# Kernel tuning notes

Measured on AMD Instinct MI355X. Metric: run time of the kernel, lower is better.

The kernel has to match this reference:

```python
import jax, jax.numpy as jnp
import numpy as np


def setup_inputs() -> dict:
    key = jax.random.key(0)
    kq, kk, kv = jax.random.split(key, 3)
    B, M, QT, KVT, H = 2, 16, 2048, 2048, 128
    q = jax.random.normal(kq, (B, M, QT, H), dtype=jnp.float32)
    k = jax.random.normal(kk, (B, M, KVT, H), dtype=jnp.float32)
    v = jax.random.normal(kv, (B, M, KVT, H), dtype=jnp.float32)
    return {"q": q, "k": k, "v": v}


def reference(q, k, v):
    # QKBmm: broadcast-multiply + sum == einsum contraction over H.
    # NOTE: original module applies NO 1/sqrt(H) scaling.
    score = jnp.einsum("bmqh,bmkh->bmqk", q, k)  # [B,M,QT,KVT]
    score = jax.nn.softmax(score, axis=-1)
    # SVBmm: broadcast-multiply + sum over KVT.
    out = jnp.einsum("bmqk,bmkh->bmqh", score, v)  # [B,M,QT,H]
    return out
```

## Files before the change

kernel.cpp:

```cpp
#include <hip/hip_runtime.h>
#include <hip/hip_bf16.h>
#include <math.h>


#define HD     128
#define QTL    2048
#define KVTL   2048
#define NHEAD  32
#define KVBLK  64
#define NKT    (KVTL / KVBLK)
#define QBLKB  128
#define TILE_BYTES 32768
#define WS_NEEDED ((size_t)NHEAD * NKT * TILE_BYTES)

using f32x4  = __attribute__((ext_vector_type(4))) float;
using f32x16 = __attribute__((ext_vector_type(16))) float;
using f16x8  = __attribute__((ext_vector_type(8))) _Float16;
using i32x2  = __attribute__((ext_vector_type(2))) int;
using i32x4  = __attribute__((ext_vector_type(4))) int;
using bf16x8 = __attribute__((ext_vector_type(8))) __bf16;
using bf16x4 = __attribute__((ext_vector_type(4))) __bf16;

#define NK_CHUNK (NHEAD * NKT * 64 * 16)
#define NV_CHUNK (NHEAD * NKT * 8 * 128)

__global__ __launch_bounds__(256) void sdpa_prep(const float* __restrict__ kg,
                                                 const float* __restrict__ vg,
                                                 char* __restrict__ ws)
{
    const int idx = blockIdx.x * 256 + threadIdx.x;
    if (idx < NK_CHUNK) {
        const int s    = idx & 15;
        const int r    = (idx >> 4) & 63;
        const int kt   = (idx >> 10) & 31;
        const int head = idx >> 15;
        const int c    = s ^ (r & 15);
        const float* src = kg + ((size_t)head * KVTL + kt * 64 + r) * HD + c * 8;
        float4 a = *(const float4*)src;
        float4 b = *(const float4*)(src + 4);
        f16x8 h8;
        h8[0] = (_Float16)a.x; h8[1] = (_Float16)a.y;
        h8[2] = (_Float16)a.z; h8[3] = (_Float16)a.w;
        h8[4] = (_Float16)b.x; h8[5] = (_Float16)b.y;
        h8[6] = (_Float16)b.z; h8[7] = (_Float16)b.w;
        char* base = ws + (size_t)(head * NKT + kt) * TILE_BYTES;
        *(f16x8*)(base + r * 256 + s * 16) = h8;
    } else if (idx < NK_CHUNK + NV_CHUNK) {
        const int j    = idx - NK_CHUNK;
        const int h    = j & 127;
        const int c    = (j >> 7) & 7;
        const int kt   = (j >> 10) & 31;
        const int head = j >> 15;
        const int rr   = h & 63;
        const int u    = h >> 6;
        const int s    = (u * 8 + c) ^ (rr & 15);
        const float* src = vg + ((size_t)head * KVTL + kt * 64 + c * 8) * HD + h;
        f16x8 o;
        #pragma unroll
        for (int i = 0; i < 8; ++i)
            o[i] = (_Float16)src[(size_t)i * HD];
        char* base = ws + (size_t)(head * NKT + kt) * TILE_BYTES;
        *(f16x8*)(base + 16384 + rr * 256 + s * 16) = o;
    }
}

__global__ __launch_bounds__(256, 2) void sdpa_fwd(const float* __restrict__ qg,
                                                   const char* __restrict__ ws,
                                                   float* __restrict__ og)
{
    const int head  = blockIdx.y;
    const int qblk  = blockIdx.x * QBLKB;
    const float* qh = qg + (size_t)head * QTL * HD;
    const char*  wh = ws + (size_t)head * NKT * TILE_BYTES;

    const int t  = threadIdx.x;
    const int wv = t >> 6;
    const int l  = t & 63;
    const int lq = l & 31;
    const int hi = l >> 5;
    const int lm = l & 15;

    __shared__ __align__(16) char arena[65536];

    f16x8 qf[8];
    {
        const float* qrow = qh + (size_t)(qblk + wv * 32 + lq) * HD;
        #pragma unroll
        for (int hs = 0; hs < 8; ++hs) {
            float4 a = *(const float4*)(qrow + hs * 16 + hi * 8);
            float4 b = *(const float4*)(qrow + hs * 16 + hi * 8 + 4);
            f16x8 f;
            f[0] = (_Float16)a.x; f[1] = (_Float16)a.y;
            f[2] = (_Float16)a.z; f[3] = (_Float16)a.w;
            f[4] = (_Float16)b.x; f[5] = (_Float16)b.y;
            f[6] = (_Float16)b.z; f[7] = (_Float16)b.w;
            qf[hs] = f;
        }
    }

    f32x16 acc_o[4];
    #pragma unroll
    for (int ht = 0; ht < 4; ++ht)
        #pragma unroll
        for (int r = 0; r < 16; ++r) acc_o[ht][r] = 0.f;

    float m = -INFINITY, ln = 0.f;
    const float LOG2E = 1.4426950408889634f;

    i32x4 stg[8];

    #pragma unroll
    for (int j = 0; j < 8; ++j)
        stg[j] = *(const i32x4*)(wh + j * 4096 + t * 16);
    #pragma unroll
    for (int j = 0; j < 8; ++j)
        *(i32x4*)(arena + j * 4096 + t * 16) = stg[j];
    __syncthreads();

    for (int kt = 0; kt < NKT; ++kt) {
        const int cur = kt & 1;
        const char* base = arena + cur * 32768;

        if (kt + 1 < NKT) {
            const char* g = wh + (size_t)(kt + 1) * TILE_BYTES;
            #pragma unroll
            for (int j = 0; j < 8; ++j)
                stg[j] = *(const i32x4*)(g + j * 4096 + t * 16);
        }

        f32x16 acc_s[2];
        __builtin_amdgcn_s_setprio(1);
        #pragma unroll
        for (int kk = 0; kk < 2; ++kk) {
            f32x16 acc;
            #pragma unroll
            for (int r = 0; r < 16; ++r) acc[r] = 0.f;
            #pragma unroll
            for (int hs = 0; hs < 8; ++hs) {
                const int off = (kk * 32 + lq) * 256 + (((hs * 2 + hi) ^ lm) * 16);
                f16x8 kf = *(const f16x8*)(base + off);
                acc = __builtin_amdgcn_mfma_f32_32x32x16_f16(kf, qf[hs], acc, 0, 0, 0);
            }
            acc_s[kk] = acc;
        }
        __builtin_amdgcn_s_setprio(0);

        float pm0 = -INFINITY, pm1 = -INFINITY, pm2 = -INFINITY, pm3 = -INFINITY;
        #pragma unroll
        for (int kk = 0; kk < 2; ++kk)
            #pragma unroll
            for (int r = 0; r < 16; r += 4) {
                pm0 = fmaxf(pm0, acc_s[kk][r + 0]);
                pm1 = fmaxf(pm1, acc_s[kk][r + 1]);
                pm2 = fmaxf(pm2, acc_s[kk][r + 2]);
                pm3 = fmaxf(pm3, acc_s[kk][r + 3]);
            }
        float pmax = fmaxf(fmaxf(pm0, pm1), fmaxf(pm2, pm3));
        pmax = fmaxf(pmax, __shfl_xor(pmax, 32));

        if (!__all(pmax <= m + 8.0f)) {
            const float mnew = fmaxf(m, pmax);
            const float sc   = exp2f((m - mnew) * LOG2E);
            m = mnew; ln *= sc;
            #pragma unroll
            for (int ht = 0; ht < 4; ++ht)
                #pragma unroll
                for (int r = 0; r < 16; ++r) acc_o[ht][r] *= sc;
        }

        i32x4 fr[4];
        #pragma unroll
        for (int kk = 0; kk < 2; ++kk) {
            float p[16];
            float s0 = 0.f, s1 = 0.f, s2 = 0.f, s3 = 0.f;
            #pragma unroll
            for (int r = 0; r < 16; r += 4) {
                p[r + 0] = exp2f((acc_s[kk][r + 0] - m) * LOG2E); s0 += p[r + 0];
                p[r + 1] = exp2f((acc_s[kk][r + 1] - m) * LOG2E); s1 += p[r + 1];
                p[r + 2] = exp2f((acc_s[kk][r + 2] - m) * LOG2E); s2 += p[r + 2];
                p[r + 3] = exp2f((acc_s[kk][r + 3] - m) * LOG2E); s3 += p[r + 3];
            }
            ln += (s0 + s1) + (s2 + s3);
            int t01 = __builtin_bit_cast(int, __builtin_amdgcn_cvt_pkrtz(p[0],  p[1]));
            int t23 = __builtin_bit_cast(int, __builtin_amdgcn_cvt_pkrtz(p[2],  p[3]));
            int t45 = __builtin_bit_cast(int, __builtin_amdgcn_cvt_pkrtz(p[4],  p[5]));
            int t67 = __builtin_bit_cast(int, __builtin_amdgcn_cvt_pkrtz(p[6],  p[7]));
            int t89 = __builtin_bit_cast(int, __builtin_amdgcn_cvt_pkrtz(p[8],  p[9]));
            int tAB = __builtin_bit_cast(int, __builtin_amdgcn_cvt_pkrtz(p[10], p[11]));
            int tCD = __builtin_bit_cast(int, __builtin_amdgcn_cvt_pkrtz(p[12], p[13]));
            int tEF = __builtin_bit_cast(int, __builtin_amdgcn_cvt_pkrtz(p[14], p[15]));
            i32x2 sw;
            sw = __builtin_amdgcn_permlane32_swap(t01, t45, false, false);
            fr[2*kk][0] = sw[0]; fr[2*kk][2] = sw[1];
            sw = __builtin_amdgcn_permlane32_swap(t23, t67, false, false);
            fr[2*kk][1] = sw[0]; fr[2*kk][3] = sw[1];
            sw = __builtin_amdgcn_permlane32_swap(t89, tCD, false, false);
            fr[2*kk+1][0] = sw[0]; fr[2*kk+1][2] = sw[1];
            sw = __builtin_amdgcn_permlane32_swap(tAB, tEF, false, false);
            fr[2*kk+1][1] = sw[0]; fr[2*kk+1][3] = sw[1];
        }

        const char* Vb = base + 16384;
        __builtin_amdgcn_s_setprio(1);
        #pragma unroll
        for (int ht = 0; ht < 4; ++ht) {
            #pragma unroll
            for (int ks = 0; ks < 4; ++ks) {
                const int off = ((ht & 1) * 32 + lq) * 256 +
                                ((((ht >> 1) * 8 + ks * 2 + hi) ^ lm) * 16);
                f16x8 vf = *(const f16x8*)(Vb + off);
                acc_o[ht] = __builtin_amdgcn_mfma_f32_32x32x16_f16(
                    vf, __builtin_bit_cast(f16x8, fr[ks]), acc_o[ht], 0, 0, 0);
            }
        }
        __builtin_amdgcn_s_setprio(0);

        if (kt + 1 < NKT) {
            char* nbuf = arena + (cur ^ 1) * 32768;
            #pragma unroll
            for (int j = 0; j < 8; ++j)
                *(i32x4*)(nbuf + j * 4096 + t * 16) = stg[j];
        }

        __syncthreads();
    }

    ln += __shfl_xor(ln, 32);
    const float inv = 1.f / ln;

    __syncthreads();
    const int qloc = wv * 32 + lq;
    #pragma unroll
    for (int ht = 0; ht < 4; ++ht) {
        #pragma unroll
        for (int r = 0; r < 4; ++r) {
            f32x4 v;
            v[0] = acc_o[ht][4*r+0] * inv;
            v[1] = acc_o[ht][4*r+1] * inv;
            v[2] = acc_o[ht][4*r+2] * inv;
            v[3] = acc_o[ht][4*r+3] * inv;
            const int slot = ht * 8 + 2 * r + hi;
            *(f32x4*)(arena + qloc * 512 + ((slot ^ lq) * 16)) = v;
        }
    }
    __syncthreads();
    {
        float* ob = og + (size_t)(head * QTL + qblk) * HD;
        #pragma unroll
        for (int j = 0; j < 16; ++j) {
            const int n  = j * 256 + t;
            const int qr = n >> 5;
            const int sl = n & 31;
            f32x4 v = *(const f32x4*)(arena + qr * 512 + ((sl ^ (qr & 31)) * 16));
            *(f32x4*)(ob + (size_t)qr * HD + sl * 4) = v;
        }
    }
}

__global__ __launch_bounds__(256) void sdpa_fwd_v1(const float* __restrict__ qg,
                                                   const float* __restrict__ kg,
                                                   const float* __restrict__ vg,
                                                   float* __restrict__ og)
{
    const int head  = blockIdx.y;
    const int qbase = blockIdx.x * 64;
    const float* qh = qg + (size_t)head * QTL * HD;
    const float* kh = kg + (size_t)head * KVTL * HD;
    const float* vh = vg + (size_t)head * KVTL * HD;
    float*       oh = og + (size_t)head * QTL * HD;

    const int t  = threadIdx.x;
    const int wv = t >> 6;
    const int l  = t & 63;
    const int lr = l & 15;
    const int lg = l >> 4;

    __shared__ __bf16 Kth[32][HD + 8];
    __shared__ __bf16 Ktl[32][HD + 8];
    __shared__ __bf16 Vt[HD][32 + 8];
    __shared__ __bf16 Pw[4][16][32 + 8];

    bf16x8 qfh[4], qfl[4];
    {
        const float* qrow = qh + (size_t)(qbase + wv * 16 + lr) * HD;
        #pragma unroll
        for (int ks = 0; ks < 4; ++ks) {
            bf16x8 fh, fl;
            #pragma unroll
            for (int i = 0; i < 8; ++i) {
                float x = qrow[ks * 32 + lg * 8 + i];
                __bf16 h = (__bf16)x;
                fh[i] = h;
                fl[i] = (__bf16)(x - (float)h);
            }
            qfh[ks] = fh; qfl[ks] = fl;
        }
    }

    f32x4 acc_o[8];
    #pragma unroll
    for (int h8 = 0; h8 < 8; ++h8) acc_o[h8] = (f32x4){0.f, 0.f, 0.f, 0.f};
    float mrow[4], lrow[4];
    #pragma unroll
    for (int r = 0; r < 4; ++r) { mrow[r] = -INFINITY; lrow[r] = 0.f; }
    const float LOG2E = 1.4426950408889634f;

    for (int kt = 0; kt < 64; ++kt) {
        const float* kbase = kh + (size_t)kt * 32 * HD;
        const float* vbase = vh + (size_t)kt * 32 * HD;
        __syncthreads();
        #pragma unroll
        for (int j = 0; j < 4; ++j) {
            const int e   = (j * 256 + t) * 4;
            const int row = e >> 7;
            const int col = e & 127;
            float4 f = *(const float4*)(kbase + e);
            bf16x4 h4, l4;
            h4[0] = (__bf16)f.x; l4[0] = (__bf16)(f.x - (float)h4[0]);
            h4[1] = (__bf16)f.y; l4[1] = (__bf16)(f.y - (float)h4[1]);
            h4[2] = (__bf16)f.z; l4[2] = (__bf16)(f.z - (float)h4[2]);
            h4[3] = (__bf16)f.w; l4[3] = (__bf16)(f.w - (float)h4[3]);
            *(bf16x4*)&Kth[row][col] = h4;
            *(bf16x4*)&Ktl[row][col] = l4;
        }
        #pragma unroll
        for (int j = 0; j < 4; ++j) {
            const int n     = t & 127;
            const int strip = (t >> 7) + 2 * j;
            bf16x4 b4;
            #pragma unroll
            for (int i = 0; i < 4; ++i)
                b4[i] = (__bf16)vbase[(size_t)(4 * strip + i) * HD + n];
            *(bf16x4*)&Vt[n][4 * strip] = b4;
        }
        __syncthreads();

        f32x4 acc_s[2];
        #pragma unroll
        for (int nt = 0; nt < 2; ++nt) {
            acc_s[nt] = (f32x4){0.f, 0.f, 0.f, 0.f};
            #pragma unroll
            for (int ks = 0; ks < 4; ++ks) {
                bf16x8 kh8 = *(const bf16x8*)&Kth[nt * 16 + lr][ks * 32 + lg * 8];
                bf16x8 kl8 = *(const bf16x8*)&Ktl[nt * 16 + lr][ks * 32 + lg * 8];
                acc_s[nt] = __builtin_amdgcn_mfma_f32_16x16x32_bf16(qfh[ks], kh8, acc_s[nt], 0, 0, 0);
                acc_s[nt] = __builtin_amdgcn_mfma_f32_16x16x32_bf16(qfl[ks], kh8, acc_s[nt], 0, 0, 0);
                acc_s[nt] = __builtin_amdgcn_mfma_f32_16x16x32_bf16(qfh[ks], kl8, acc_s[nt], 0, 0, 0);
            }
        }
        float p[2][4];
        #pragma unroll
        for (int r = 0; r < 4; ++r) {
            float vm = fmaxf(acc_s[0][r], acc_s[1][r]);
            vm = fmaxf(vm, __shfl_xor(vm, 1));
            vm = fmaxf(vm, __shfl_xor(vm, 2));
            vm = fmaxf(vm, __shfl_xor(vm, 4));
            vm = fmaxf(vm, __shfl_xor(vm, 8));
            const float mnew  = fmaxf(mrow[r], vm);
            const float scale = exp2f((mrow[r] - mnew) * LOG2E);
            mrow[r] = mnew;
            float ps = 0.f;
            #pragma unroll
            for (int nt = 0; nt < 2; ++nt) {
                float pe = exp2f((acc_s[nt][r] - mnew) * LOG2E);
                p[nt][r] = pe; ps += pe;
            }
            lrow[r] = lrow[r] * scale + ps;
            #pragma unroll
            for (int h8 = 0; h8 < 8; ++h8) acc_o[h8][r] *= scale;
        }
        #pragma unroll
        for (int nt = 0; nt < 2; ++nt)
            #pragma unroll
            for (int r = 0; r < 4; ++r)
                Pw[wv][lg * 4 + r][nt * 16 + lr] = (__bf16)p[nt][r];
        bf16x8 pf = *(const bf16x8*)&Pw[wv][lr][lg * 8];
        #pragma unroll
        for (int h8 = 0; h8 < 8; ++h8) {
            bf16x8 vf = *(const bf16x8*)&Vt[h8 * 16 + lr][lg * 8];
            acc_o[h8] = __builtin_amdgcn_mfma_f32_16x16x32_bf16(pf, vf, acc_o[h8], 0, 0, 0);
        }
    }
    float invl[4];
    #pragma unroll
    for (int r = 0; r < 4; ++r) {
        float s = lrow[r];
        s += __shfl_xor(s, 1);
        s += __shfl_xor(s, 2);
        s += __shfl_xor(s, 4);
        s += __shfl_xor(s, 8);
        invl[r] = 1.f / s;
    }
    float* ob = oh + (size_t)(qbase + wv * 16) * HD;
    #pragma unroll
    for (int h8 = 0; h8 < 8; ++h8)
        #pragma unroll
        for (int r = 0; r < 4; ++r)
            ob[(size_t)(lg * 4 + r) * HD + h8 * 16 + lr] = acc_o[h8][r] * invl[r];
}

extern "C" void kernel_launch(void* const* d_in, const int* in_sizes, int n_in,
                              void* d_out, int out_size, void* d_ws, size_t ws_size,
                              hipStream_t stream) {
    const float* q = (const float*)d_in[0];
    const float* k = (const float*)d_in[1];
    const float* v = (const float*)d_in[2];
    float* out = (float*)d_out;

    if (ws_size >= WS_NEEDED) {
        char* ws = (char*)d_ws;
        const int total_chunks = NK_CHUNK + NV_CHUNK;
        sdpa_prep<<<total_chunks / 256, 256, 0, stream>>>(k, v, ws);
        dim3 grid(QTL / QBLKB, NHEAD, 1);
        sdpa_fwd<<<grid, dim3(256, 1, 1), 0, stream>>>(q, ws, out);
    } else {
        dim3 grid(QTL / 64, NHEAD, 1);
        sdpa_fwd_v1<<<grid, dim3(256, 1, 1), 0, stream>>>(q, k, v, out);
    }
}
```

Measured before the change: 115.9 us.

## Use 512-thread blocks over 256 query rows with 128-key double-buffered tiles

Each block now has 8 waves covering 256 query rows, where before it had 4 waves over 128 rows. Each loop iteration stages a 128-key K/V tile (two 64-key subtiles) into 128KB of double-buffered dynamic LDS, and the online softmax runs per 32-key chunk inside the iteration. This halves both the number of times each K/V tile is copied from global memory into LDS and the number of block barriers per key. In exchange, occupancy drops to one large block per CU with only 256 blocks in the grid. It also relies on the device accepting a 128KB dynamic shared-memory launch.

```diff
diff --git a/kernel.cpp b/kernel.cpp
--- a/kernel.cpp
+++ b/kernel.cpp
@@ -7,11 +7,12 @@
 #define QTL    2048
 #define KVTL   2048
 #define NHEAD  32
-#define KVBLK  64
-#define NKT    (KVTL / KVBLK)
-#define QBLKB  128
-#define TILE_BYTES 32768
-#define WS_NEEDED ((size_t)NHEAD * NKT * TILE_BYTES)
+#define NKT64  32
+#define NITER  16
+#define QBLKB  256
+#define SUB_BYTES  32768
+#define TILE2_BYTES 65536
+#define WS_NEEDED ((size_t)NHEAD * NKT64 * SUB_BYTES)
 
 using f32x4  = __attribute__((ext_vector_type(4))) float;
 using f32x16 = __attribute__((ext_vector_type(16))) float;
@@ -21,8 +22,8 @@
 using bf16x8 = __attribute__((ext_vector_type(8))) __bf16;
 using bf16x4 = __attribute__((ext_vector_type(4))) __bf16;
 
-#define NK_CHUNK (NHEAD * NKT * 64 * 16)
-#define NV_CHUNK (NHEAD * NKT * 8 * 128)
+#define NK_CHUNK (NHEAD * NKT64 * 64 * 16)
+#define NV_CHUNK (NHEAD * NKT64 * 8 * 128)
 
 __global__ __launch_bounds__(256) void sdpa_prep(const float* __restrict__ kg,
                                                  const float* __restrict__ vg,
@@ -43,7 +44,7 @@
         h8[2] = (_Float16)a.z; h8[3] = (_Float16)a.w;
         h8[4] = (_Float16)b.x; h8[5] = (_Float16)b.y;
         h8[6] = (_Float16)b.z; h8[7] = (_Float16)b.w;
-        char* base = ws + (size_t)(head * NKT + kt) * TILE_BYTES;
+        char* base = ws + (size_t)(head * NKT64 + kt) * SUB_BYTES;
         *(f16x8*)(base + r * 256 + s * 16) = h8;
     } else if (idx < NK_CHUNK + NV_CHUNK) {
         const int j    = idx - NK_CHUNK;
@@ -59,19 +60,21 @@
         #pragma unroll
         for (int i = 0; i < 8; ++i)
             o[i] = (_Float16)src[(size_t)i * HD];
-        char* base = ws + (size_t)(head * NKT + kt) * TILE_BYTES;
+        char* base = ws + (size_t)(head * NKT64 + kt) * SUB_BYTES;
         *(f16x8*)(base + 16384 + rr * 256 + s * 16) = o;
     }
 }
 
-__global__ __launch_bounds__(256, 2) void sdpa_fwd(const float* __restrict__ qg,
+__global__ __launch_bounds__(512, 1) void sdpa_fwd(const float* __restrict__ qg,
                                                    const char* __restrict__ ws,
                                                    float* __restrict__ og)
 {
+    extern __shared__ __align__(16) char arena[];
+
     const int head  = blockIdx.y;
     const int qblk  = blockIdx.x * QBLKB;
     const float* qh = qg + (size_t)head * QTL * HD;
-    const char*  wh = ws + (size_t)head * NKT * TILE_BYTES;
+    const char*  wh = ws + (size_t)head * NKT64 * SUB_BYTES;
 
     const int t  = threadIdx.x;
     const int wv = t >> 6;
@@ -79,8 +82,6 @@
     const int lq = l & 31;
     const int hi = l >> 5;
     const int lm = l & 15;
-
-    __shared__ __align__(16) char arena[65536];
 
     f16x8 qf[8];
     {
@@ -108,118 +109,111 @@
     const float LOG2E = 1.4426950408889634f;
 
     i32x4 stg[8];
-
     #pragma unroll
     for (int j = 0; j < 8; ++j)
-        stg[j] = *(const i32x4*)(wh + j * 4096 + t * 16);
+        stg[j] = *(const i32x4*)(wh + j * 8192 + t * 16);
     #pragma unroll
     for (int j = 0; j < 8; ++j)
-        *(i32x4*)(arena + j * 4096 + t * 16) = stg[j];
+        *(i32x4*)(arena + j * 8192 + t * 16) = stg[j];
     __syncthreads();
 
-    for (int kt = 0; kt < NKT; ++kt) {
+    for (int kt = 0; kt < NITER; ++kt) {
         const int cur = kt & 1;
-        const char* base = arena + cur * 32768;
-
-        if (kt + 1 < NKT) {
-            const char* g = wh + (size_t)(kt + 1) * TILE_BYTES;
+        const char* base = arena + cur * TILE2_BYTES;
+
+        if (kt + 1 < NITER) {
+            const char* g = wh + (size_t)(kt + 1) * TILE2_BYTES;
             #pragma unroll
             for (int j = 0; j < 8; ++j)
-                stg[j] = *(const i32x4*)(g + j * 4096 + t * 16);
-        }
-
-        f32x16 acc_s[2];
-        __builtin_amdgcn_s_setprio(1);
-        #pragma unroll
-        for (int kk = 0; kk < 2; ++kk) {
-            f32x16 acc;
-            #pragma unroll
-            for (int r = 0; r < 16; ++r) acc[r] = 0.f;
+                stg[j] = *(const i32x4*)(g + j * 8192 + t * 16);
+        }
+
+        #pragma unroll
+        for (int kk = 0; kk < 4; ++kk) {
+            const char* sub = base + (kk >> 1) * SUB_BYTES;
+
+            f32x16 acc_s;
+            #pragma unroll
+            for (int r = 0; r < 16; ++r) acc_s[r] = 0.f;
+            __builtin_amdgcn_s_setprio(1);
             #pragma unroll
             for (int hs = 0; hs < 8; ++hs) {
-                const int off = (kk * 32 + lq) * 256 + (((hs * 2 + hi) ^ lm) * 16);
-                f16x8 kf = *(const f16x8*)(base + off);
-                acc = __builtin_amdgcn_mfma_f32_32x32x16_f16(kf, qf[hs], acc, 0, 0, 0);
-            }
-            acc_s[kk] = acc;
-        }
-        __builtin_amdgcn_s_setprio(0);
-
-        float pm0 = -INFINITY, pm1 = -INFINITY, pm2 = -INFINITY, pm3 = -INFINITY;
-        #pragma unroll
-        for (int kk = 0; kk < 2; ++kk)
-            #pragma unroll
-            for (int r = 0; r < 16; r += 4) {
-                pm0 = fmaxf(pm0, acc_s[kk][r + 0]);
-                pm1 = fmaxf(pm1, acc_s[kk][r + 1]);
-                pm2 = fmaxf(pm2, acc_s[kk][r + 2]);
-                pm3 = fmaxf(pm3, acc_s[kk][r + 3]);
-            }
-        float pmax = fmaxf(fmaxf(pm0, pm1), fmaxf(pm2, pm3));
-        pmax = fmaxf(pmax, __shfl_xor(pmax, 32));
-
-        if (!__all(pmax <= m + 8.0f)) {
-            const float mnew = fmaxf(m, pmax);
-            const float sc   = exp2f((m - mnew) * LOG2E);
-            m = mnew; ln *= sc;
-            #pragma unroll
-            for (int ht = 0; ht < 4; ++ht)
+                const int off = ((kk & 1) * 32 + lq) * 256 + (((hs * 2 + hi) ^ lm) * 16);
+                f16x8 kf = *(const f16x8*)(sub + off);
+                acc_s = __builtin_amdgcn_mfma_f32_32x32x16_f16(kf, qf[hs], acc_s, 0, 0, 0);
+            }
+            __builtin_amdgcn_s_setprio(0);
+
+            float pm0 = fmaxf(fmaxf(acc_s[0], acc_s[1]), fmaxf(acc_s[2], acc_s[3]));
+            float pm1 = fmaxf(fmaxf(acc_s[4], acc_s[5]), fmaxf(acc_s[6], acc_s[7]));
+            float pm2 = fmaxf(fmaxf(acc_s[8], acc_s[9]), fmaxf(acc_s[10], acc_s[11]));
+            float pm3 = fmaxf(fmaxf(acc_s[12], acc_s[13]), fmaxf(acc_s[14], acc_s[15]));
+            float pmax = fmaxf(fmaxf(pm0, pm1), fmaxf(pm2, pm3));
+            pmax = fmaxf(pmax, __shfl_xor(pmax, 32));
+            if (!__all(pmax <= m + 8.0f)) {
+                const float mnew = fmaxf(m, pmax);
+                const float sc   = exp2f((m - mnew) * LOG2E);
+                m = mnew; ln *= sc;
                 #pragma unroll
-                for (int r = 0; r < 16; ++r) acc_o[ht][r] *= sc;
-        }
-
-        i32x4 fr[4];
-        #pragma unroll
-        for (int kk = 0; kk < 2; ++kk) {
+                for (int ht = 0; ht < 4; ++ht)
+                    #pragma unroll
+                    for (int r = 0; r < 16; ++r) acc_o[ht][r] *= sc;
+            }
+
             float p[16];
-            float s0 = 0.f, s1 = 0.f, s2 = 0.f, s3 = 0.f;
-            #pragma unroll
-            for (int r = 0; r < 16; r += 4) {
-                p[r + 0] = exp2f((acc_s[kk][r + 0] - m) * LOG2E); s0 += p[r + 0];
-                p[r + 1] = exp2f((acc_s[kk][r + 1] - m) * LOG2E); s1 += p[r + 1];
-                p[r + 2] = exp2f((acc_s[kk][r + 2] - m) * LOG2E); s2 += p[r + 2];
-                p[r + 3] = exp2f((acc_s[kk][r + 3] - m) * LOG2E); s3 += p[r + 3];
-            }
-            ln += (s0 + s1) + (s2 + s3);
-            int t01 = __builtin_bit_cast(int, __builtin_amdgcn_cvt_pkrtz(p[0],  p[1]));
-            int t23 = __builtin_bit_cast(int, __builtin_amdgcn_cvt_pkrtz(p[2],  p[3]));
-            int t45 = __builtin_bit_cast(int, __builtin_amdgcn_cvt_pkrtz(p[4],  p[5]));
-            int t67 = __builtin_bit_cast(int, __builtin_amdgcn_cvt_pkrtz(p[6],  p[7]));
-            int t89 = __builtin_bit_cast(int, __builtin_amdgcn_cvt_pkrtz(p[8],  p[9]));
-            int tAB = __builtin_bit_cast(int, __builtin_amdgcn_cvt_pkrtz(p[10], p[11]));
-            int tCD = __builtin_bit_cast(int, __builtin_amdgcn_cvt_pkrtz(p[12], p[13]));
-            int tEF = __builtin_bit_cast(int, __builtin_amdgcn_cvt_pkrtz(p[14], p[15]));
-            i32x2 sw;
-            sw = __builtin_amdgcn_permlane32_swap(t01, t45, false, false);
-            fr[2*kk][0] = sw[0]; fr[2*kk][2] = sw[1];
-            sw = __builtin_amdgcn_permlane32_swap(t23, t67, false, false);
-            fr[2*kk][1] = sw[0]; fr[2*kk][3] = sw[1];
-            sw = __builtin_amdgcn_permlane32_swap(t89, tCD, false, false);
-            fr[2*kk+1][0] = sw[0]; fr[2*kk+1][2] = sw[1];
-            sw = __builtin_amdgcn_permlane32_swap(tAB, tEF, false, false);
-            fr[2*kk+1][1] = sw[0]; fr[2*kk+1][3] = sw[1];
-        }
-
-        const char* Vb = base + 16384;
-        __builtin_amdgcn_s_setprio(1);
-        #pragma unroll
-        for (int ht = 0; ht < 4; ++ht) {
-            #pragma unroll
-            for (int ks = 0; ks < 4; ++ks) {
-                const int off = ((ht & 1) * 32 + lq) * 256 +
-                                ((((ht >> 1) * 8 + ks * 2 + hi) ^ lm) * 16);
-                f16x8 vf = *(const f16x8*)(Vb + off);
-                acc_o[ht] = __builtin_amdgcn_mfma_f32_32x32x16_f16(
-                    vf, __builtin_bit_cast(f16x8, fr[ks]), acc_o[ht], 0, 0, 0);
-            }
-        }
-        __builtin_amdgcn_s_setprio(0);
-
-        if (kt + 1 < NKT) {
-            char* nbuf = arena + (cur ^ 1) * 32768;
+            {
+                float s0 = 0.f, s1 = 0.f, s2 = 0.f, s3 = 0.f;
+                #pragma unroll
+                for (int r = 0; r < 16; r += 4) {
+                    p[r + 0] = exp2f((acc_s[r + 0] - m) * LOG2E); s0 += p[r + 0];
+                    p[r + 1] = exp2f((acc_s[r + 1] - m) * LOG2E); s1 += p[r + 1];
+                    p[r + 2] = exp2f((acc_s[r + 2] - m) * LOG2E); s2 += p[r + 2];
+                    p[r + 3] = exp2f((acc_s[r + 3] - m) * LOG2E); s3 += p[r + 3];
+                }
+                ln += (s0 + s1) + (s2 + s3);
+            }
+            i32x4 fr[2];
+            {
+                int t01 = __builtin_bit_cast(int, __builtin_amdgcn_cvt_pkrtz(p[0],  p[1]));
+                int t23 = __builtin_bit_cast(int, __builtin_amdgcn_cvt_pkrtz(p[2],  p[3]));
+                int t45 = __builtin_bit_cast(int, __builtin_amdgcn_cvt_pkrtz(p[4],  p[5]));
+                int t67 = __builtin_bit_cast(int, __builtin_amdgcn_cvt_pkrtz(p[6],  p[7]));
+                int t89 = __builtin_bit_cast(int, __builtin_amdgcn_cvt_pkrtz(p[8],  p[9]));
+                int tAB = __builtin_bit_cast(int, __builtin_amdgcn_cvt_pkrtz(p[10], p[11]));
+                int tCD = __builtin_bit_cast(int, __builtin_amdgcn_cvt_pkrtz(p[12], p[13]));
+                int tEF = __builtin_bit_cast(int, __builtin_amdgcn_cvt_pkrtz(p[14], p[15]));
+                i32x2 sw;
+                sw = __builtin_amdgcn_permlane32_swap(t01, t45, false, false);
+                fr[0][0] = sw[0]; fr[0][2] = sw[1];
+                sw = __builtin_amdgcn_permlane32_swap(t23, t67, false, false);
+                fr[0][1] = sw[0]; fr[0][3] = sw[1];
+                sw = __builtin_amdgcn_permlane32_swap(t89, tCD, false, false);
+                fr[1][0] = sw[0]; fr[1][2] = sw[1];
+                sw = __builtin_amdgcn_permlane32_swap(tAB, tEF, false, false);
+                fr[1][1] = sw[0]; fr[1][3] = sw[1];
+            }
+
+            const char* Vb = sub + 16384;
+            __builtin_amdgcn_s_setprio(1);
+            #pragma unroll
+            for (int ht = 0; ht < 4; ++ht) {
+                #pragma unroll
+                for (int ks = 0; ks < 2; ++ks) {
+                    const int mm = (ht >> 1) * 8 + (kk & 1) * 4 + ks * 2 + hi;
+                    const int off = ((ht & 1) * 32 + lq) * 256 + ((mm ^ lm) * 16);
+                    f16x8 vf = *(const f16x8*)(Vb + off);
+                    acc_o[ht] = __builtin_amdgcn_mfma_f32_32x32x16_f16(
+                        vf, __builtin_bit_cast(f16x8, fr[ks]), acc_o[ht], 0, 0, 0);
+                }
+            }
+            __builtin_amdgcn_s_setprio(0);
+        }
+
+        if (kt + 1 < NITER) {
+            char* nbuf = arena + (cur ^ 1) * TILE2_BYTES;
             #pragma unroll
             for (int j = 0; j < 8; ++j)
-                *(i32x4*)(nbuf + j * 4096 + t * 16) = stg[j];
+                *(i32x4*)(nbuf + j * 8192 + t * 16) = stg[j];
         }
 
         __syncthreads();
@@ -248,7 +242,7 @@
         float* ob = og + (size_t)(head * QTL + qblk) * HD;
         #pragma unroll
         for (int j = 0; j < 16; ++j) {
-            const int n  = j * 256 + t;
+            const int n  = j * 512 + t;
             const int qr = n >> 5;
             const int sl = n & 31;
             f32x4 v = *(const f32x4*)(arena + qr * 512 + ((sl ^ (qr & 31)) * 16));
@@ -412,7 +406,7 @@
         const int total_chunks = NK_CHUNK + NV_CHUNK;
         sdpa_prep<<<total_chunks / 256, 256, 0, stream>>>(k, v, ws);
         dim3 grid(QTL / QBLKB, NHEAD, 1);
-        sdpa_fwd<<<grid, dim3(256, 1, 1), 0, stream>>>(q, ws, out);
+        sdpa_fwd<<<grid, dim3(512, 1, 1), 131072, stream>>>(q, ws, out);
     } else {
         dim3 grid(QTL / 64, NHEAD, 1);
         sdpa_fwd_v1<<<grid, dim3(256, 1, 1), 0, stream>>>(q, k, v, out);
```

Result: slower. 123.3 us (+6.3%).
